# Performance work log

Hardware: AMD Instinct MI355X
Metric: run time of the kernel (lower is better)

Reference implementation:

```python
import jax, jax.numpy as jnp
import numpy as np

NUM_STAGES = 3
EPS = 1e-6


def _l2norm(x, axis):
    return x / (EPS + jnp.linalg.norm(x, axis=axis, keepdims=True))


def _l1norm(x, axis):
    return x / (EPS + jnp.sum(x, axis=axis, keepdims=True))


def setup_inputs() -> dict:
    key = jax.random.key(0)
    k1, k2 = jax.random.split(key)
    B, C, H, W, K = 16, 512, 64, 64, 64
    feats = jax.random.normal(k1, (B, C, H, W), dtype=jnp.float32)
    # bases buffer: N(0, sqrt(2/K)) then l2-normalized along channel dim (done in reference)
    bases = jax.random.normal(k2, (1, C, K), dtype=jnp.float32) * np.sqrt(2.0 / K)
    return {"feats": feats, "bases": bases}


def reference(feats, bases):
    B, C, H, W = feats.shape
    f = feats.reshape(B, C, H * W)              # [B, C, N]
    b = _l2norm(bases, axis=1)                  # match buffer init normalization
    b = jnp.broadcast_to(b, (B, C, b.shape[2])) # [B, C, K]
    attention = None
    for _ in range(NUM_STAGES):
        attention = jnp.einsum('bcn,bck->bnk', f, b)        # [B, N, K]
        attention = jax.nn.softmax(attention, axis=2)
        attention_normed = _l1norm(attention, axis=1)
        b = jnp.einsum('bcn,bnk->bck', f, attention_normed)  # [B, C, K]
        b = _l2norm(b, axis=1)
    # EM loop runs under torch.no_grad in the original
    b = jax.lax.stop_gradient(b)
    attention = jax.lax.stop_gradient(attention)
    feats_recon = jnp.einsum('bck,bnk->bcn', b, attention)   # [B, C, N]
    return feats_recon.reshape(B, C, H, W)
```

## Files before the change

### kernel.cpp

```cpp
#include <hip/hip_runtime.h>
#include <stdint.h>

#define B_ 16
#define C_ 512
#define N_ 4096
#define K_ 64
#define NUM_STAGES 3

typedef __bf16 bf16x8 __attribute__((ext_vector_type(8)));
typedef float f32x4 __attribute__((ext_vector_type(4)));

__device__ __forceinline__ uint16_t f2bf(float x) {
  union { float f; uint32_t u; } v; v.f = x;
  uint32_t r = (v.u + 0x7FFFu + ((v.u >> 16) & 1u)) >> 16;
  return (uint16_t)r;
}

__device__ __forceinline__ void async16(const uint16_t* g, uint16_t* l) {
  __builtin_amdgcn_global_load_lds(
      (const __attribute__((address_space(1))) unsigned int*)g,
      (__attribute__((address_space(3))) unsigned int*)l, 16, 0, 0);
}

__global__ __launch_bounds__(256) void k_prep(const float* __restrict__ feats,
                                              uint16_t* __restrict__ f16,
                                              uint16_t* __restrict__ fT16) {
  __shared__ uint16_t tile[64][68];
  int b = blockIdx.z, c0 = blockIdx.y * 64, n0 = blockIdx.x * 256;
  int t = threadIdx.x;
  int cl = t >> 4;
  int nl = (t & 15) * 4;
  for (int nt = 0; nt < 4; ++nt) {
    int n0s = n0 + nt * 64;
    const float* src = feats + ((size_t)b * C_ + c0) * N_ + n0s;
    uint16_t* dst = f16 + ((size_t)b * C_ + c0) * N_ + n0s;
    __syncthreads();
#pragma unroll
    for (int i = 0; i < 4; ++i) {
      int c = cl + 16 * i;
      float4 v = *(const float4*)(src + (size_t)c * N_ + nl);
      ushort4 x;
      x.x = f2bf(v.x); x.y = f2bf(v.y); x.z = f2bf(v.z); x.w = f2bf(v.w);
      *(ushort4*)(dst + (size_t)c * N_ + nl) = x;
      *(ushort4*)&tile[c][nl] = x;
    }
    __syncthreads();
    uint16_t* dstT = fT16 + ((size_t)b * N_ + n0s) * C_ + c0;
#pragma unroll
    for (int i = 0; i < 4; ++i) {
      int n = cl + 16 * i;
      int c = nl;
      ushort4 y;
      y.x = tile[c + 0][n]; y.y = tile[c + 1][n];
      y.z = tile[c + 2][n]; y.w = tile[c + 3][n];
      *(ushort4*)(dstT + (size_t)n * C_ + c) = y;
    }
  }
}

__global__ __launch_bounds__(256) void k_init_basis(const float* __restrict__ bases,
                                                    uint16_t* __restrict__ basis,
                                                    uint16_t* __restrict__ basisT) {
  int b = blockIdx.x;
  int t = threadIdx.x;
  __shared__ float red[256];
  __shared__ float inv[64];
  int k = t & 63;
  float s = 0.f;
  for (int c = (t >> 6); c < C_; c += 4) {
    float v = bases[c * K_ + k];
    s += v * v;
  }
  red[t] = s;
  __syncthreads();
  if (t < 64) {
    float tot = red[t] + red[t + 64] + red[t + 128] + red[t + 192];
    inv[t] = 1.f / (1e-6f + sqrtf(tot));
  }
  __syncthreads();
  uint16_t* ob = basis + (size_t)b * C_ * K_;
  for (int i = 0; i < (C_ * K_) / 256; ++i) {
    int idx = t + 256 * i;
    int kk = idx & 63;
    ob[idx] = f2bf(bases[idx] * inv[kk]);
  }
  uint16_t* obT = basisT + (size_t)b * K_ * C_;
  for (int i = 0; i < (C_ * K_) / 256; ++i) {
    int idx = t + 256 * i;
    int kk = idx >> 9;
    int cc = idx & 511;
    obT[idx] = f2bf(bases[cc * K_ + kk] * inv[kk]);
  }
}

__global__ __launch_bounds__(512) void k_gemm1(const uint16_t* __restrict__ fT,
                                               const uint16_t* __restrict__ basisT,
                                               uint16_t* __restrict__ attn,
                                               uint16_t* __restrict__ attnT,
                                               int write_attn) {
  __shared__ __attribute__((aligned(16))) uint16_t ldsA[128 * 64];
  __shared__ __attribute__((aligned(16))) uint16_t ldsB[64 * 64];
  int b = blockIdx.y;
  int n0 = blockIdx.x * 128;
  int t = threadIdx.x;
  int w = t >> 6, lane = t & 63, l15 = lane & 15, quad = lane >> 4;
  const uint16_t* A = fT + ((size_t)b * N_ + n0) * C_;
  const uint16_t* Bm = basisT + (size_t)b * K_ * C_;
  f32x4 acc[4] = {};
  for (int cs = 0; cs < C_; cs += 64) {
    __syncthreads();
#pragma unroll
    for (int r = 0; r < 2; ++r) {
      int e = r * 512 + t;
      int row = e >> 3, ch = e & 7;
      int sch = (ch + row) & 7;
      async16(A + (size_t)row * C_ + cs + sch * 8, ldsA + (r * 512 + (t & 448)) * 8);
    }
    {
      int row = t >> 3, ch = t & 7;
      int sch = (ch + row) & 7;
      async16(Bm + (size_t)row * C_ + cs + sch * 8, ldsB + (t & 448) * 8);
    }
    __syncthreads();
#pragma unroll
    for (int s = 0; s < 2; ++s) {
      int cc = s * 4 + quad;
      int ra = 16 * w + l15;
      bf16x8 af = *(const bf16x8*)(ldsA + ra * 64 + ((cc - ra) & 7) * 8);
#pragma unroll
      for (int t4 = 0; t4 < 4; ++t4) {
        int rb = 16 * t4 + l15;
        bf16x8 bv = *(const bf16x8*)(ldsB + rb * 64 + ((cc - rb) & 7) * 8);
        acc[t4] = __builtin_amdgcn_mfma_f32_16x16x32_bf16(af, bv, acc[t4], 0, 0, 0);
      }
    }
  }
  float p[4][4];
#pragma unroll
  for (int r = 0; r < 4; ++r) {
    float m = fmaxf(fmaxf(acc[0][r], acc[1][r]), fmaxf(acc[2][r], acc[3][r]));
    m = fmaxf(m, __shfl_xor(m, 1));
    m = fmaxf(m, __shfl_xor(m, 2));
    m = fmaxf(m, __shfl_xor(m, 4));
    m = fmaxf(m, __shfl_xor(m, 8));
    float s = 0.f;
#pragma unroll
    for (int t4 = 0; t4 < 4; ++t4) { p[t4][r] = __expf(acc[t4][r] - m); s += p[t4][r]; }
    s += __shfl_xor(s, 1); s += __shfl_xor(s, 2);
    s += __shfl_xor(s, 4); s += __shfl_xor(s, 8);
    float inv = 1.f / s;
#pragma unroll
    for (int t4 = 0; t4 < 4; ++t4) p[t4][r] *= inv;
  }
  if (write_attn) {
    uint16_t* oa = attn + ((size_t)b * N_ + n0 + 16 * w + quad * 4) * K_;
#pragma unroll
    for (int r = 0; r < 4; ++r) {
#pragma unroll
      for (int t4 = 0; t4 < 4; ++t4) oa[(size_t)r * K_ + 16 * t4 + l15] = f2bf(p[t4][r]);
    }
  }
#pragma unroll
  for (int t4 = 0; t4 < 4; ++t4) {
    ushort4 y;
    y.x = f2bf(p[t4][0]); y.y = f2bf(p[t4][1]);
    y.z = f2bf(p[t4][2]); y.w = f2bf(p[t4][3]);
    *(ushort4*)(attnT + ((size_t)b * K_ + 16 * t4 + l15) * N_ + n0 + 16 * w + quad * 4) = y;
  }
}

__global__ __launch_bounds__(512) void k_gemm2(const uint16_t* __restrict__ f16,
                                               const uint16_t* __restrict__ attnT,
                                               float* __restrict__ brawT) {
  __shared__ __attribute__((aligned(16))) uint16_t ldsF[128 * 64];
  __shared__ __attribute__((aligned(16))) uint16_t ldsP[64 * 64];
  int b = blockIdx.z;
  int slice = blockIdx.y;
  int c0 = blockIdx.x * 128;
  int t = threadIdx.x;
  int w = t >> 6, lane = t & 63, l15 = lane & 15, quad = lane >> 4;
  const uint16_t* F = f16 + ((size_t)b * C_ + c0) * N_;
  const uint16_t* P = attnT + (size_t)b * K_ * N_;
  f32x4 acc[4] = {};
  int ns0 = slice * 512;
  for (int ns = ns0; ns < ns0 + 512; ns += 64) {
    __syncthreads();
#pragma unroll
    for (int r = 0; r < 2; ++r) {
      int e = r * 512 + t;
      int row = e >> 3, ch = e & 7;
      int sch = (ch + row) & 7;
      async16(F + (size_t)row * N_ + ns + sch * 8, ldsF + (r * 512 + (t & 448)) * 8);
    }
    {
      int row = t >> 3, ch = t & 7;
      int sch = (ch + row) & 7;
      async16(P + (size_t)row * N_ + ns + sch * 8, ldsP + (t & 448) * 8);
    }
    __syncthreads();
#pragma unroll
    for (int s = 0; s < 2; ++s) {
      int cc = s * 4 + quad;
      int rb = 16 * w + l15;
      bf16x8 fv = *(const bf16x8*)(ldsF + rb * 64 + ((cc - rb) & 7) * 8);
#pragma unroll
      for (int kt = 0; kt < 4; ++kt) {
        int ra = 16 * kt + l15;
        bf16x8 av = *(const bf16x8*)(ldsP + ra * 64 + ((cc - ra) & 7) * 8);
        acc[kt] = __builtin_amdgcn_mfma_f32_16x16x32_bf16(av, fv, acc[kt], 0, 0, 0);
      }
    }
  }
  float* outp = brawT + ((size_t)slice * B_ + b) * K_ * C_;
#pragma unroll
  for (int kt = 0; kt < 4; ++kt) {
#pragma unroll
    for (int r = 0; r < 4; ++r) {
      outp[(size_t)(16 * kt + quad * 4 + r) * C_ + c0 + 16 * w + l15] = acc[kt][r];
    }
  }
}

__global__ __launch_bounds__(256) void k_l2norm(const float* __restrict__ brawT,
                                                uint16_t* __restrict__ basisT) {
  int b = blockIdx.x;
  int t = threadIdx.x, w = t >> 6, lane = t & 63;
  for (int k = w; k < K_; k += 4) {
    float v[8];
#pragma unroll
    for (int j = 0; j < 8; ++j) v[j] = 0.f;
#pragma unroll
    for (int s = 0; s < 8; ++s) {
      const float* rs = brawT + (((size_t)s * B_ + b) * K_ + k) * C_ + lane * 8;
      float4 a = *(const float4*)(rs);
      float4 c4 = *(const float4*)(rs + 4);
      v[0] += a.x; v[1] += a.y; v[2] += a.z; v[3] += a.w;
      v[4] += c4.x; v[5] += c4.y; v[6] += c4.z; v[7] += c4.w;
    }
    float ss = 0.f;
#pragma unroll
    for (int j = 0; j < 8; ++j) ss += v[j] * v[j];
    ss += __shfl_xor(ss, 1); ss += __shfl_xor(ss, 2); ss += __shfl_xor(ss, 4);
    ss += __shfl_xor(ss, 8); ss += __shfl_xor(ss, 16); ss += __shfl_xor(ss, 32);
    float inv = 1.f / (1e-6f + sqrtf(ss));
    ushort4 y0, y1;
    y0.x = f2bf(v[0] * inv); y0.y = f2bf(v[1] * inv);
    y0.z = f2bf(v[2] * inv); y0.w = f2bf(v[3] * inv);
    y1.x = f2bf(v[4] * inv); y1.y = f2bf(v[5] * inv);
    y1.z = f2bf(v[6] * inv); y1.w = f2bf(v[7] * inv);
    uint16_t* o = basisT + ((size_t)b * K_ + k) * C_ + lane * 8;
    *(ushort4*)(o) = y0;
    *(ushort4*)(o + 4) = y1;
  }
}

__global__ __launch_bounds__(256) void k_transpose_basis(const uint16_t* __restrict__ basisT,
                                                         uint16_t* __restrict__ basis) {
  __shared__ uint16_t tile[64][65];
  int b = blockIdx.y, ct = blockIdx.x;
  int t = threadIdx.x;
  const uint16_t* src = basisT + (size_t)b * K_ * C_ + ct * 64;
  for (int i = 0; i < 16; ++i) {
    int idx = t + 256 * i;
    int k = idx >> 6, c = idx & 63;
    tile[k][c] = src[(size_t)k * C_ + c];
  }
  __syncthreads();
  uint16_t* dst = basis + (size_t)b * C_ * K_ + (size_t)ct * 64 * K_;
  for (int i = 0; i < 16; ++i) {
    int idx = t + 256 * i;
    int c = idx >> 6, k = idx & 63;
    dst[(size_t)c * K_ + k] = tile[k][c];
  }
}

__global__ __launch_bounds__(512) void k_recon(const uint16_t* __restrict__ attn,
                                               const uint16_t* __restrict__ basis,
                                               float* __restrict__ out) {
  __shared__ __attribute__((aligned(16))) uint16_t ldsA[128 * 64];
  __shared__ __attribute__((aligned(16))) uint16_t ldsB[64 * 64];
  int b = blockIdx.z, c0 = blockIdx.y * 64, n0 = blockIdx.x * 128;
  int t = threadIdx.x, w = t >> 6, lane = t & 63, l15 = lane & 15, quad = lane >> 4;
  const uint16_t* A = attn + ((size_t)b * N_ + n0) * K_;
  const uint16_t* Bm = basis + ((size_t)b * C_ + c0) * K_;
#pragma unroll
  for (int r = 0; r < 2; ++r) {
    int e = r * 512 + t;
    int row = e >> 3, ch = e & 7, sch = (ch + row) & 7;
    async16(A + (size_t)row * K_ + sch * 8, ldsA + (r * 512 + (t & 448)) * 8);
  }
  {
    int row = t >> 3, ch = t & 7, sch = (ch + row) & 7;
    async16(Bm + (size_t)row * K_ + sch * 8, ldsB + (t & 448) * 8);
  }
  f32x4 acc[4] = {};
  __syncthreads();
#pragma unroll
  for (int s = 0; s < 2; ++s) {
    int cc = s * 4 + quad;
    int ra = 16 * w + l15;
    bf16x8 af = *(const bf16x8*)(ldsA + ra * 64 + ((cc - ra) & 7) * 8);
#pragma unroll
    for (int t4 = 0; t4 < 4; ++t4) {
      int rb = 16 * t4 + l15;
      bf16x8 bv = *(const bf16x8*)(ldsB + rb * 64 + ((cc - rb) & 7) * 8);
      acc[t4] = __builtin_amdgcn_mfma_f32_16x16x32_bf16(af, bv, acc[t4], 0, 0, 0);
    }
  }
#pragma unroll
  for (int t4 = 0; t4 < 4; ++t4) {
    int c = c0 + 16 * t4 + l15;
    float4 v = make_float4(acc[t4][0], acc[t4][1], acc[t4][2], acc[t4][3]);
    *(float4*)(out + ((size_t)b * C_ + c) * N_ + n0 + 16 * w + quad * 4) = v;
  }
}

extern "C" void kernel_launch(void* const* d_in, const int* in_sizes, int n_in,
                              void* d_out, int out_size, void* d_ws, size_t ws_size,
                              hipStream_t stream) {
  const float* feats = (const float*)d_in[0];
  const float* bases = (const float*)d_in[1];
  float* out = (float*)d_out;
  char* ws = (char*)d_ws;
  uint16_t* f16 = (uint16_t*)(ws);
  uint16_t* fT16 = (uint16_t*)(ws + 67108864);
  uint16_t* attn = (uint16_t*)(ws + 134217728);
  uint16_t* attnT = (uint16_t*)(ws + 142606336);
  uint16_t* basis = (uint16_t*)(ws + 150994944);
  uint16_t* basisT = (uint16_t*)(ws + 152043520);
  float* brawT = (float*)(ws + 153092096);

  k_prep<<<dim3(16, 8, 16), 256, 0, stream>>>(feats, f16, fT16);
  k_init_basis<<<16, 256, 0, stream>>>(bases, basis, basisT);
  for (int st = 0; st < NUM_STAGES; ++st) {
    k_gemm1<<<dim3(32, 16), 512, 0, stream>>>(fT16, basisT, attn, attnT,
                                              st == NUM_STAGES - 1 ? 1 : 0);
    k_gemm2<<<dim3(4, 8, 16), 512, 0, stream>>>(f16, attnT, brawT);
    k_l2norm<<<16, 256, 0, stream>>>(brawT, basisT);
    k_transpose_basis<<<dim3(8, 16), 256, 0, stream>>>(basisT, basis);
  }
  k_recon<<<dim3(32, 8, 16), 512, 0, stream>>>(attn, basis, out);
}
```

Measured before the change: 507.4 us.

## Enlarge GEMM K-tiles, split gemm2 finer, fuse basis transpose into l2norm, retile prep

Both GEMMs now stage 256-wide reduction chunks in dynamic LDS (96 KB), so there are fewer barrier and load rounds. gemm2 is split into 16 N-slices, each handled in a single load pass, which doubles its grid. The l2norm kernel runs over a (batch, k-group) grid, sums the 16 partial slices, and writes both basisT and the transposed basis, so the separate transpose kernel is dropped. The prep kernel uses one 64x64 tile per block with a padded tile. The price is much larger LDS per block, which lowers occupancy, plus strided scalar writes for basis.

```diff
diff --git a/kernel.cpp b/kernel.cpp
--- a/kernel.cpp
+++ b/kernel.cpp
@@ -25,36 +25,33 @@
 __global__ __launch_bounds__(256) void k_prep(const float* __restrict__ feats,
                                               uint16_t* __restrict__ f16,
                                               uint16_t* __restrict__ fT16) {
-  __shared__ uint16_t tile[64][68];
-  int b = blockIdx.z, c0 = blockIdx.y * 64, n0 = blockIdx.x * 256;
+  __shared__ uint16_t tile[64][65];
+  int b = blockIdx.z, c0 = blockIdx.y * 64, n0 = blockIdx.x * 64;
   int t = threadIdx.x;
+  const float* src = feats + ((size_t)b * C_ + c0) * N_ + n0;
+  uint16_t* dst = f16 + ((size_t)b * C_ + c0) * N_ + n0;
   int cl = t >> 4;
   int nl = (t & 15) * 4;
-  for (int nt = 0; nt < 4; ++nt) {
-    int n0s = n0 + nt * 64;
-    const float* src = feats + ((size_t)b * C_ + c0) * N_ + n0s;
-    uint16_t* dst = f16 + ((size_t)b * C_ + c0) * N_ + n0s;
-    __syncthreads();
-#pragma unroll
-    for (int i = 0; i < 4; ++i) {
-      int c = cl + 16 * i;
-      float4 v = *(const float4*)(src + (size_t)c * N_ + nl);
-      ushort4 x;
-      x.x = f2bf(v.x); x.y = f2bf(v.y); x.z = f2bf(v.z); x.w = f2bf(v.w);
-      *(ushort4*)(dst + (size_t)c * N_ + nl) = x;
-      *(ushort4*)&tile[c][nl] = x;
-    }
-    __syncthreads();
-    uint16_t* dstT = fT16 + ((size_t)b * N_ + n0s) * C_ + c0;
-#pragma unroll
-    for (int i = 0; i < 4; ++i) {
-      int n = cl + 16 * i;
-      int c = nl;
-      ushort4 y;
-      y.x = tile[c + 0][n]; y.y = tile[c + 1][n];
-      y.z = tile[c + 2][n]; y.w = tile[c + 3][n];
-      *(ushort4*)(dstT + (size_t)n * C_ + c) = y;
-    }
+#pragma unroll
+  for (int i = 0; i < 4; ++i) {
+    int c = cl + 16 * i;
+    float4 v = *(const float4*)(src + (size_t)c * N_ + nl);
+    ushort4 x;
+    x.x = f2bf(v.x); x.y = f2bf(v.y); x.z = f2bf(v.z); x.w = f2bf(v.w);
+    *(ushort4*)(dst + (size_t)c * N_ + nl) = x;
+    tile[c][nl + 0] = x.x; tile[c][nl + 1] = x.y;
+    tile[c][nl + 2] = x.z; tile[c][nl + 3] = x.w;
+  }
+  __syncthreads();
+  uint16_t* dstT = fT16 + ((size_t)b * N_ + n0) * C_ + c0;
+#pragma unroll
+  for (int i = 0; i < 4; ++i) {
+    int n = cl + 16 * i;
+    int c = nl;
+    ushort4 y;
+    y.x = tile[c + 0][n]; y.y = tile[c + 1][n];
+    y.z = tile[c + 2][n]; y.w = tile[c + 3][n];
+    *(ushort4*)(dstT + (size_t)n * C_ + c) = y;
   }
 }
 
@@ -98,8 +95,9 @@
                                                uint16_t* __restrict__ attn,
                                                uint16_t* __restrict__ attnT,
                                                int write_attn) {
-  __shared__ __attribute__((aligned(16))) uint16_t ldsA[128 * 64];
-  __shared__ __attribute__((aligned(16))) uint16_t ldsB[64 * 64];
+  extern __shared__ __attribute__((aligned(16))) uint16_t lds[];
+  uint16_t* ldsA = lds;
+  uint16_t* ldsB = lds + 128 * 256;
   int b = blockIdx.y;
   int n0 = blockIdx.x * 128;
   int t = threadIdx.x;
@@ -107,31 +105,34 @@
   const uint16_t* A = fT + ((size_t)b * N_ + n0) * C_;
   const uint16_t* Bm = basisT + (size_t)b * K_ * C_;
   f32x4 acc[4] = {};
-  for (int cs = 0; cs < C_; cs += 64) {
+  for (int h = 0; h < 2; ++h) {
+    int c0h = h * 256;
     __syncthreads();
 #pragma unroll
-    for (int r = 0; r < 2; ++r) {
-      int e = r * 512 + t;
-      int row = e >> 3, ch = e & 7;
-      int sch = (ch + row) & 7;
-      async16(A + (size_t)row * C_ + cs + sch * 8, ldsA + (r * 512 + (t & 448)) * 8);
-    }
-    {
-      int row = t >> 3, ch = t & 7;
-      int sch = (ch + row) & 7;
-      async16(Bm + (size_t)row * C_ + cs + sch * 8, ldsB + (t & 448) * 8);
+    for (int i = 0; i < 8; ++i) {
+      int e = i * 512 + t;
+      int row = e >> 5, ch = e & 31;
+      async16(A + (size_t)row * C_ + c0h + ((ch + row) & 31) * 8,
+              ldsA + (i * 512 + (t & 448)) * 8);
+    }
+#pragma unroll
+    for (int i = 0; i < 4; ++i) {
+      int e = i * 512 + t;
+      int row = e >> 5, ch = e & 31;
+      async16(Bm + (size_t)row * C_ + c0h + ((ch + row) & 31) * 8,
+              ldsB + (i * 512 + (t & 448)) * 8);
     }
     __syncthreads();
 #pragma unroll
-    for (int s = 0; s < 2; ++s) {
-      int cc = s * 4 + quad;
+    for (int s = 0; s < 8; ++s) {
+      int g = s * 4 + quad;
       int ra = 16 * w + l15;
-      bf16x8 af = *(const bf16x8*)(ldsA + ra * 64 + ((cc - ra) & 7) * 8);
-#pragma unroll
-      for (int t4 = 0; t4 < 4; ++t4) {
-        int rb = 16 * t4 + l15;
-        bf16x8 bv = *(const bf16x8*)(ldsB + rb * 64 + ((cc - rb) & 7) * 8);
-        acc[t4] = __builtin_amdgcn_mfma_f32_16x16x32_bf16(af, bv, acc[t4], 0, 0, 0);
+      bf16x8 af = *(const bf16x8*)(ldsA + ((size_t)ra * 32 + ((g - ra) & 31)) * 8);
+#pragma unroll
+      for (int kt = 0; kt < 4; ++kt) {
+        int rb = 16 * kt + l15;
+        bf16x8 bv = *(const bf16x8*)(ldsB + ((size_t)rb * 32 + ((g - rb) & 31)) * 8);
+        acc[kt] = __builtin_amdgcn_mfma_f32_16x16x32_bf16(af, bv, acc[kt], 0, 0, 0);
       }
     }
   }
@@ -145,70 +146,70 @@
     m = fmaxf(m, __shfl_xor(m, 8));
     float s = 0.f;
 #pragma unroll
-    for (int t4 = 0; t4 < 4; ++t4) { p[t4][r] = __expf(acc[t4][r] - m); s += p[t4][r]; }
+    for (int kt = 0; kt < 4; ++kt) { p[kt][r] = __expf(acc[kt][r] - m); s += p[kt][r]; }
     s += __shfl_xor(s, 1); s += __shfl_xor(s, 2);
     s += __shfl_xor(s, 4); s += __shfl_xor(s, 8);
     float inv = 1.f / s;
 #pragma unroll
-    for (int t4 = 0; t4 < 4; ++t4) p[t4][r] *= inv;
+    for (int kt = 0; kt < 4; ++kt) p[kt][r] *= inv;
   }
   if (write_attn) {
     uint16_t* oa = attn + ((size_t)b * N_ + n0 + 16 * w + quad * 4) * K_;
 #pragma unroll
     for (int r = 0; r < 4; ++r) {
 #pragma unroll
-      for (int t4 = 0; t4 < 4; ++t4) oa[(size_t)r * K_ + 16 * t4 + l15] = f2bf(p[t4][r]);
-    }
-  }
-#pragma unroll
-  for (int t4 = 0; t4 < 4; ++t4) {
+      for (int kt = 0; kt < 4; ++kt) oa[(size_t)r * K_ + 16 * kt + l15] = f2bf(p[kt][r]);
+    }
+  }
+#pragma unroll
+  for (int kt = 0; kt < 4; ++kt) {
     ushort4 y;
-    y.x = f2bf(p[t4][0]); y.y = f2bf(p[t4][1]);
-    y.z = f2bf(p[t4][2]); y.w = f2bf(p[t4][3]);
-    *(ushort4*)(attnT + ((size_t)b * K_ + 16 * t4 + l15) * N_ + n0 + 16 * w + quad * 4) = y;
+    y.x = f2bf(p[kt][0]); y.y = f2bf(p[kt][1]);
+    y.z = f2bf(p[kt][2]); y.w = f2bf(p[kt][3]);
+    *(ushort4*)(attnT + ((size_t)b * K_ + 16 * kt + l15) * N_ + n0 + 16 * w + quad * 4) = y;
   }
 }
 
 __global__ __launch_bounds__(512) void k_gemm2(const uint16_t* __restrict__ f16,
                                                const uint16_t* __restrict__ attnT,
                                                float* __restrict__ brawT) {
-  __shared__ __attribute__((aligned(16))) uint16_t ldsF[128 * 64];
-  __shared__ __attribute__((aligned(16))) uint16_t ldsP[64 * 64];
+  extern __shared__ __attribute__((aligned(16))) uint16_t lds[];
+  uint16_t* ldsF = lds;
+  uint16_t* ldsP = lds + 128 * 256;
   int b = blockIdx.z;
   int slice = blockIdx.y;
   int c0 = blockIdx.x * 128;
+  int ns0 = slice * 256;
   int t = threadIdx.x;
   int w = t >> 6, lane = t & 63, l15 = lane & 15, quad = lane >> 4;
-  const uint16_t* F = f16 + ((size_t)b * C_ + c0) * N_;
-  const uint16_t* P = attnT + (size_t)b * K_ * N_;
+  const uint16_t* F = f16 + ((size_t)b * C_ + c0) * N_ + ns0;
+  const uint16_t* P = attnT + (size_t)b * K_ * N_ + ns0;
+#pragma unroll
+  for (int i = 0; i < 8; ++i) {
+    int e = i * 512 + t;
+    int row = e >> 5, ch = e & 31;
+    async16(F + (size_t)row * N_ + ((ch + row) & 31) * 8,
+            ldsF + (i * 512 + (t & 448)) * 8);
+  }
+#pragma unroll
+  for (int i = 0; i < 4; ++i) {
+    int e = i * 512 + t;
+    int row = e >> 5, ch = e & 31;
+    async16(P + (size_t)row * N_ + ((ch + row) & 31) * 8,
+            ldsP + (i * 512 + (t & 448)) * 8);
+  }
   f32x4 acc[4] = {};
-  int ns0 = slice * 512;
-  for (int ns = ns0; ns < ns0 + 512; ns += 64) {
-    __syncthreads();
-#pragma unroll
-    for (int r = 0; r < 2; ++r) {
-      int e = r * 512 + t;
-      int row = e >> 3, ch = e & 7;
-      int sch = (ch + row) & 7;
-      async16(F + (size_t)row * N_ + ns + sch * 8, ldsF + (r * 512 + (t & 448)) * 8);
-    }
-    {
-      int row = t >> 3, ch = t & 7;
-      int sch = (ch + row) & 7;
-      async16(P + (size_t)row * N_ + ns + sch * 8, ldsP + (t & 448) * 8);
-    }
-    __syncthreads();
-#pragma unroll
-    for (int s = 0; s < 2; ++s) {
-      int cc = s * 4 + quad;
-      int rb = 16 * w + l15;
-      bf16x8 fv = *(const bf16x8*)(ldsF + rb * 64 + ((cc - rb) & 7) * 8);
-#pragma unroll
-      for (int kt = 0; kt < 4; ++kt) {
-        int ra = 16 * kt + l15;
-        bf16x8 av = *(const bf16x8*)(ldsP + ra * 64 + ((cc - ra) & 7) * 8);
-        acc[kt] = __builtin_amdgcn_mfma_f32_16x16x32_bf16(av, fv, acc[kt], 0, 0, 0);
-      }
+  __syncthreads();
+#pragma unroll
+  for (int s = 0; s < 8; ++s) {
+    int g = s * 4 + quad;
+    int rc = 16 * w + l15;
+    bf16x8 fv = *(const bf16x8*)(ldsF + ((size_t)rc * 32 + ((g - rc) & 31)) * 8);
+#pragma unroll
+    for (int kt = 0; kt < 4; ++kt) {
+      int ra = 16 * kt + l15;
+      bf16x8 av = *(const bf16x8*)(ldsP + ((size_t)ra * 32 + ((g - ra) & 31)) * 8);
+      acc[kt] = __builtin_amdgcn_mfma_f32_16x16x32_bf16(av, fv, acc[kt], 0, 0, 0);
     }
   }
   float* outp = brawT + ((size_t)slice * B_ + b) * K_ * C_;
@@ -222,56 +223,37 @@
 }
 
 __global__ __launch_bounds__(256) void k_l2norm(const float* __restrict__ brawT,
-                                                uint16_t* __restrict__ basisT) {
-  int b = blockIdx.x;
+                                                uint16_t* __restrict__ basisT,
+                                                uint16_t* __restrict__ basis) {
+  int b = blockIdx.x, kg = blockIdx.y;
   int t = threadIdx.x, w = t >> 6, lane = t & 63;
-  for (int k = w; k < K_; k += 4) {
-    float v[8];
-#pragma unroll
-    for (int j = 0; j < 8; ++j) v[j] = 0.f;
-#pragma unroll
-    for (int s = 0; s < 8; ++s) {
-      const float* rs = brawT + (((size_t)s * B_ + b) * K_ + k) * C_ + lane * 8;
-      float4 a = *(const float4*)(rs);
-      float4 c4 = *(const float4*)(rs + 4);
-      v[0] += a.x; v[1] += a.y; v[2] += a.z; v[3] += a.w;
-      v[4] += c4.x; v[5] += c4.y; v[6] += c4.z; v[7] += c4.w;
-    }
-    float ss = 0.f;
-#pragma unroll
-    for (int j = 0; j < 8; ++j) ss += v[j] * v[j];
-    ss += __shfl_xor(ss, 1); ss += __shfl_xor(ss, 2); ss += __shfl_xor(ss, 4);
-    ss += __shfl_xor(ss, 8); ss += __shfl_xor(ss, 16); ss += __shfl_xor(ss, 32);
-    float inv = 1.f / (1e-6f + sqrtf(ss));
-    ushort4 y0, y1;
-    y0.x = f2bf(v[0] * inv); y0.y = f2bf(v[1] * inv);
-    y0.z = f2bf(v[2] * inv); y0.w = f2bf(v[3] * inv);
-    y1.x = f2bf(v[4] * inv); y1.y = f2bf(v[5] * inv);
-    y1.z = f2bf(v[6] * inv); y1.w = f2bf(v[7] * inv);
-    uint16_t* o = basisT + ((size_t)b * K_ + k) * C_ + lane * 8;
-    *(ushort4*)(o) = y0;
-    *(ushort4*)(o + 4) = y1;
-  }
-}
-
-__global__ __launch_bounds__(256) void k_transpose_basis(const uint16_t* __restrict__ basisT,
-                                                         uint16_t* __restrict__ basis) {
-  __shared__ uint16_t tile[64][65];
-  int b = blockIdx.y, ct = blockIdx.x;
-  int t = threadIdx.x;
-  const uint16_t* src = basisT + (size_t)b * K_ * C_ + ct * 64;
-  for (int i = 0; i < 16; ++i) {
-    int idx = t + 256 * i;
-    int k = idx >> 6, c = idx & 63;
-    tile[k][c] = src[(size_t)k * C_ + c];
-  }
-  __syncthreads();
-  uint16_t* dst = basis + (size_t)b * C_ * K_ + (size_t)ct * 64 * K_;
-  for (int i = 0; i < 16; ++i) {
-    int idx = t + 256 * i;
-    int c = idx >> 6, k = idx & 63;
-    dst[(size_t)c * K_ + k] = tile[k][c];
-  }
+  int k = kg * 4 + w;
+  float v[8];
+#pragma unroll
+  for (int j = 0; j < 8; ++j) v[j] = 0.f;
+#pragma unroll
+  for (int s = 0; s < 16; ++s) {
+    const float* rs = brawT + (((size_t)s * B_ + b) * K_ + k) * C_ + lane * 8;
+    float4 a = *(const float4*)(rs);
+    float4 c4 = *(const float4*)(rs + 4);
+    v[0] += a.x; v[1] += a.y; v[2] += a.z; v[3] += a.w;
+    v[4] += c4.x; v[5] += c4.y; v[6] += c4.z; v[7] += c4.w;
+  }
+  float ss = 0.f;
+#pragma unroll
+  for (int j = 0; j < 8; ++j) ss += v[j] * v[j];
+  ss += __shfl_xor(ss, 1); ss += __shfl_xor(ss, 2); ss += __shfl_xor(ss, 4);
+  ss += __shfl_xor(ss, 8); ss += __shfl_xor(ss, 16); ss += __shfl_xor(ss, 32);
+  float inv = 1.f / (1e-6f + sqrtf(ss));
+  uint16_t y[8];
+#pragma unroll
+  for (int j = 0; j < 8; ++j) y[j] = f2bf(v[j] * inv);
+  uint16_t* o = basisT + ((size_t)b * K_ + k) * C_ + lane * 8;
+  *(ushort4*)(o) = *(ushort4*)&y[0];
+  *(ushort4*)(o + 4) = *(ushort4*)&y[4];
+  uint16_t* ob = basis + (size_t)b * C_ * K_ + k;
+#pragma unroll
+  for (int j = 0; j < 8; ++j) ob[(size_t)(lane * 8 + j) * K_] = y[j];
 }
 
 __global__ __launch_bounds__(512) void k_recon(const uint16_t* __restrict__ attn,
@@ -299,11 +281,11 @@
   for (int s = 0; s < 2; ++s) {
     int cc = s * 4 + quad;
     int ra = 16 * w + l15;
-    bf16x8 af = *(const bf16x8*)(ldsA + ra * 64 + ((cc - ra) & 7) * 8);
+    bf16x8 af = *(const bf16x8*)(ldsA + (ra * 8 + ((cc - ra) & 7)) * 8);
 #pragma unroll
     for (int t4 = 0; t4 < 4; ++t4) {
       int rb = 16 * t4 + l15;
-      bf16x8 bv = *(const bf16x8*)(ldsB + rb * 64 + ((cc - rb) & 7) * 8);
+      bf16x8 bv = *(const bf16x8*)(ldsB + (rb * 8 + ((cc - rb) & 7)) * 8);
       acc[t4] = __builtin_amdgcn_mfma_f32_16x16x32_bf16(af, bv, acc[t4], 0, 0, 0);
     }
   }
@@ -330,14 +312,19 @@
   uint16_t* basisT = (uint16_t*)(ws + 152043520);
   float* brawT = (float*)(ws + 153092096);
 
-  k_prep<<<dim3(16, 8, 16), 256, 0, stream>>>(feats, f16, fT16);
+  const int ldsBytes = (128 * 256 + 64 * 256) * 2;
+  (void)hipFuncSetAttribute((const void*)k_gemm1,
+                            hipFuncAttributeMaxDynamicSharedMemorySize, ldsBytes);
+  (void)hipFuncSetAttribute((const void*)k_gemm2,
+                            hipFuncAttributeMaxDynamicSharedMemorySize, ldsBytes);
+
+  k_prep<<<dim3(64, 8, 16), 256, 0, stream>>>(feats, f16, fT16);
   k_init_basis<<<16, 256, 0, stream>>>(bases, basis, basisT);
   for (int st = 0; st < NUM_STAGES; ++st) {
-    k_gemm1<<<dim3(32, 16), 512, 0, stream>>>(fT16, basisT, attn, attnT,
-                                              st == NUM_STAGES - 1 ? 1 : 0);
-    k_gemm2<<<dim3(4, 8, 16), 512, 0, stream>>>(f16, attnT, brawT);
-    k_l2norm<<<16, 256, 0, stream>>>(brawT, basisT);
-    k_transpose_basis<<<dim3(8, 16), 256, 0, stream>>>(basisT, basis);
+    k_gemm1<<<dim3(32, 16), 512, ldsBytes, stream>>>(fT16, basisT, attn, attnT,
+                                                     st == NUM_STAGES - 1 ? 1 : 0);
+    k_gemm2<<<dim3(4, 16, 16), 512, ldsBytes, stream>>>(f16, attnT, brawT);
+    k_l2norm<<<dim3(16, 16), 256, 0, stream>>>(brawT, basisT, basis);
   }
   k_recon<<<dim3(32, 8, 16), 512, 0, stream>>>(attn, basis, out);
 }
```

New measurement: 491.3 us. 3.2% less time.
